# Performance work log

Hardware: AMD Instinct MI355X
Metric: run time of the kernel (lower is better)

Reference implementation:

```python
import jax, jax.numpy as jnp
import numpy as np

B, N, D = 2, 128, 512  # batch, tokens, embed_dim (= in_features = out_features)
LAYERS = 3


def setup_inputs() -> dict:
    key = jax.random.key(0)
    ks = jax.random.split(key, 9)
    s = lambda fan_in: 1.0 / np.sqrt(fan_in)
    return {
        "text_embedding": jax.random.normal(ks[0], (B, N, D), dtype=jnp.float32),
        # weights stored as [in, out] so y = x @ W + b (matches torch Linear math)
        "W_rel": jax.random.uniform(ks[1], (2 * D, D), jnp.float32, -s(2 * D), s(2 * D)),
        "b_rel": jax.random.uniform(ks[2], (D,), jnp.float32, -s(2 * D), s(2 * D)),
        "W_go": jax.random.uniform(ks[3], (D, D), jnp.float32, -s(D), s(D)),
        "b_go": jax.random.uniform(ks[4], (D,), jnp.float32, -s(D), s(D)),
        "W_gr": jax.random.uniform(ks[5], (3 * D, D), jnp.float32, -s(3 * D), s(3 * D)),
        "b_gr": jax.random.uniform(ks[6], (D,), jnp.float32, -s(3 * D), s(3 * D)),
        "W_esa": jax.random.uniform(ks[7], (D, D), jnp.float32, -s(D), s(D)),
        "b_esa": jax.random.uniform(ks[8], (D,), jnp.float32, -s(D), s(D)),
    }


def reference(text_embedding, W_rel, b_rel, W_go, b_go, W_gr, b_gr, W_esa, b_esa):
    x = text_embedding  # [B, N, D]
    n = x.shape[1]
    rel = None
    for i in range(LAYERS):
        new_x = jnp.tanh(x @ W_go + b_go)  # [B, N, D]
        # pairwise broadcast-concat: [B, N, N, 2D]
        a = jnp.broadcast_to(x[:, :, None, :], (x.shape[0], n, n, x.shape[-1]))
        b = jnp.broadcast_to(x[:, None, :, :], (x.shape[0], n, n, x.shape[-1]))
        rlf = jnp.concatenate([a, b], axis=3)
        if i == 0:
            rel = rlf @ W_rel + b_rel  # [B, N, N, D]
        rlf2 = jnp.concatenate([rlf, rel], axis=3)  # [B, N, N, 3D]
        rel = jnp.tanh(rlf2 @ W_gr + b_gr)  # [B, N, N, D]
        x = new_x
    rel = rel @ W_esa + b_esa  # [B, N, N, D]
    # original subtracts max over dim=1 then applies Softmax(dim=1); equivalent to stable softmax over axis 1
    attn = jax.nn.softmax(rel, axis=1)
    rel_out = jnp.sum(attn * rel, axis=-2)  # sum over second N axis -> [B, N, D]
    return (x, rel_out)
```

## Files before the change

kernel.cpp:

```cpp
#include <hip/hip_runtime.h>
#include <hip/hip_bf16.h>
#include <stdint.h>


#define DEV static __device__ __forceinline__

typedef float  f32x4   __attribute__((ext_vector_type(4)));
typedef float  f32x16  __attribute__((ext_vector_type(16)));
typedef __bf16 bf16x8  __attribute__((ext_vector_type(8)));
typedef __bf16 bf16x4  __attribute__((ext_vector_type(4)));

DEV float tanh_fast(float x) {
  float e = __expf(2.0f * x);
  return 1.0f - 2.0f * __frcp_rn(e + 1.0f);
}

DEV void gl_lds16(const void* g, void* l) {
  __builtin_amdgcn_global_load_lds(
      (const __attribute__((address_space(1))) unsigned int*)g,
      (__attribute__((address_space(3))) unsigned int*)l, 16, 0, 0);
}

struct WC { const float* W; __bf16* Wh; __bf16* Wl; };
struct Prep {
  WC w[7];
  const float* x0; __bf16* x0h; __bf16* x0l;
  const float* b_rel; const float* Wgrc; const float* b_gr; float* dvec;
};

__global__ __launch_bounds__(256) void prep_kernel(Prep pp) {
  const int y = blockIdx.y;
  if (y < 7) {
    const WC wc = pp.w[y];
    __shared__ float tile[32][33];
    int t = threadIdx.x;
    int tx = t & 31, ty = t >> 5;
    int bx = blockIdx.x & 15, by = blockIdx.x >> 4;
    int k0 = by * 32, n0 = bx * 32;
#pragma unroll
    for (int r = 0; r < 4; ++r) {
      int k = ty + r * 8;
      tile[k][tx] = wc.W[(size_t)(k0 + k) * 512 + n0 + tx];
    }
    __syncthreads();
#pragma unroll
    for (int r = 0; r < 4; ++r) {
      int n = ty + r * 8;
      float v = tile[tx][n];
      __bf16 h = (__bf16)v;
      wc.Wh[(size_t)(n0 + n) * 512 + k0 + tx] = h;
      wc.Wl[(size_t)(n0 + n) * 512 + k0 + tx] = (__bf16)(v - (float)h);
    }
  } else if (y == 7) {
    int i = blockIdx.x * 256 + threadIdx.x;
    if (i < 32768) {
      float4 v = ((const float4*)pp.x0)[i];
      float vv[4] = {v.x, v.y, v.z, v.w};
      bf16x4 h, l;
#pragma unroll
      for (int e = 0; e < 4; ++e) {
        __bf16 he = (__bf16)vv[e];
        h[e] = he;
        l[e] = (__bf16)(vv[e] - (float)he);
      }
      ((bf16x4*)pp.x0h)[i] = h;
      ((bf16x4*)pp.x0l)[i] = l;
    }
  } else {
    if (blockIdx.x < 2) {
      int n = blockIdx.x * 256 + threadIdx.x;
      float acc = pp.b_gr[n];
#pragma unroll 8
      for (int k = 0; k < 512; ++k) acc += pp.b_rel[k] * pp.Wgrc[(size_t)k * 512 + n];
      pp.dvec[n] = acc;
    }
  }
}

struct MOp {
  const __bf16* Xh; const __bf16* Xl;
  const __bf16* Wh; const __bf16* Wl;
  const float* bias;
  const float* add;
  float* outf;
  __bf16* outh; __bf16* outl;
  int act;
};
struct MBatch { MOp op[5]; };

__global__ __launch_bounds__(256, 2) void mfma_small_kernel(MBatch batch) {
  const MOp o = batch.op[blockIdx.y];
  const int m0 = ((int)blockIdx.x >> 3) * 64;
  const int n0 = ((int)blockIdx.x & 7) * 64;
  __shared__ __bf16 Ah[64 * 64], Al[64 * 64], Bh[64 * 64], Bl[64 * 64];
  const int t = threadIdx.x, lane = t & 63, wave = t >> 6;
  const int waveM = wave >> 1, waveN = wave & 1;
  const bool comp = (o.Xl != nullptr);

  f32x4 vzero = {0.f, 0.f, 0.f, 0.f};
  f32x4 acc[2][2];
#pragma unroll
  for (int a = 0; a < 2; ++a)
#pragma unroll
    for (int c = 0; c < 2; ++c) acc[a][c] = vzero;

  const int lr = lane >> 3, lc = (lane & 7) * 8;

  for (int k0 = 0; k0 < 512; k0 += 64) {
    __syncthreads();
#pragma unroll
    for (int r = 0; r < 2; ++r) {
      const int rb = r * 32 + wave * 8;
      gl_lds16(o.Xh + (size_t)(m0 + rb + lr) * 512 + k0 + lc, &Ah[rb * 64]);
      gl_lds16(o.Wh + (size_t)(n0 + rb + lr) * 512 + k0 + lc, &Bh[rb * 64]);
      if (comp) {
        gl_lds16(o.Xl + (size_t)(m0 + rb + lr) * 512 + k0 + lc, &Al[rb * 64]);
        gl_lds16(o.Wl + (size_t)(n0 + rb + lr) * 512 + k0 + lc, &Bl[rb * 64]);
      }
    }
    __syncthreads();
#pragma unroll
    for (int kk = 0; kk < 2; ++kk) {
      const int koff = kk * 32 + (lane >> 4) * 8;
      const int ml = lane & 15;
      bf16x8 ah[2], bh[2], al[2], bl[2];
#pragma unroll
      for (int tm = 0; tm < 2; ++tm)
        ah[tm] = *(const bf16x8*)&Ah[(waveM * 32 + tm * 16 + ml) * 64 + koff];
#pragma unroll
      for (int tn = 0; tn < 2; ++tn)
        bh[tn] = *(const bf16x8*)&Bh[(waveN * 32 + tn * 16 + ml) * 64 + koff];
      if (comp) {
#pragma unroll
        for (int tm = 0; tm < 2; ++tm)
          al[tm] = *(const bf16x8*)&Al[(waveM * 32 + tm * 16 + ml) * 64 + koff];
#pragma unroll
        for (int tn = 0; tn < 2; ++tn)
          bl[tn] = *(const bf16x8*)&Bl[(waveN * 32 + tn * 16 + ml) * 64 + koff];
      }
#pragma unroll
      for (int tm = 0; tm < 2; ++tm)
#pragma unroll
        for (int tn = 0; tn < 2; ++tn) {
          acc[tm][tn] = __builtin_amdgcn_mfma_f32_16x16x32_bf16(ah[tm], bh[tn], acc[tm][tn], 0, 0, 0);
          if (comp) {
            acc[tm][tn] = __builtin_amdgcn_mfma_f32_16x16x32_bf16(ah[tm], bl[tn], acc[tm][tn], 0, 0, 0);
            acc[tm][tn] = __builtin_amdgcn_mfma_f32_16x16x32_bf16(al[tm], bh[tn], acc[tm][tn], 0, 0, 0);
          }
        }
    }
  }

  const int quad = lane >> 4, cl = lane & 15;
#pragma unroll
  for (int tm = 0; tm < 2; ++tm) {
#pragma unroll
    for (int r = 0; r < 4; ++r) {
      const int row = m0 + waveM * 32 + tm * 16 + quad * 4 + r;
#pragma unroll
      for (int tn = 0; tn < 2; ++tn) {
        const int col = n0 + waveN * 32 + tn * 16 + cl;
        float v = acc[tm][tn][r];
        if (o.bias) v += o.bias[col];
        if (o.add) v += o.add[(size_t)row * 512 + col];
        if (o.act) v = tanh_fast(v);
        if (o.outf) o.outf[(size_t)row * 512 + col] = v;
        if (o.outh) {
          __bf16 h = (__bf16)v;
          o.outh[(size_t)row * 512 + col] = h;
          o.outl[(size_t)row * 512 + col] = (__bf16)(v - (float)h);
        }
      }
    }
  }
}

__global__ __launch_bounds__(256) void rel1_kernel(
    const float* __restrict__ A, const float* __restrict__ C,
    __bf16* __restrict__ R1) {
  size_t e = ((size_t)blockIdx.x * 256 + threadIdx.x) * 8;
  int d = (int)(e & 511);
  int j = (int)((e >> 9) & 127);
  int bi = (int)(e >> 16);
  int b = bi >> 7;
  const float* ap = &A[(size_t)bi * 512 + d];
  const float* cp = &C[((size_t)(b * 128 + j)) * 512 + d];
  float av[8], cv[8];
  *(float4*)&av[0] = *(const float4*)ap;
  *(float4*)&av[4] = *(const float4*)(ap + 4);
  *(float4*)&cv[0] = *(const float4*)cp;
  *(float4*)&cv[4] = *(const float4*)(cp + 4);
  bf16x8 o;
#pragma unroll
  for (int k = 0; k < 8; ++k) o[k] = (__bf16)tanh_fast(av[k] + cv[k]);
  *(bf16x8*)&R1[e] = o;
}

constexpr int BM = 128, BN = 128, BK = 64;
DEV int lds_off(int row) { return row * 64 + (row >> 3) * 8; }

template <int MODE>
__global__ __launch_bounds__(256, 2) void big_gemm_kernel(
    const __bf16* __restrict__ Ab, const __bf16* __restrict__ Wt,
    const float* __restrict__ P, const float* __restrict__ Q,
    const float* __restrict__ bias, __bf16* __restrict__ outb,
    float* __restrict__ outf) {
  __shared__ __bf16 As[BM * BK + 16 * 8];
  __shared__ __bf16 Bs[BN * BK + 16 * 8];
  const int t = threadIdx.x;
  const int lane = t & 63;
  const int wave = t >> 6;
  const int bm = (int)blockIdx.x >> 2;
  const int n0 = ((int)blockIdx.x & 3) * BN;
  const size_t r0 = (size_t)bm * BM;
  const int b = bm >> 7;
  const int i = bm & 127;
  const int waveM = wave >> 1, waveN = wave & 1;

  f32x16 acc[2][2];
#pragma unroll
  for (int a = 0; a < 2; ++a)
#pragma unroll
    for (int c = 0; c < 2; ++c) acc[a][c] = (f32x16)0.f;

  for (int k0 = 0; k0 < 512; k0 += BK) {
    __syncthreads();
#pragma unroll
    for (int p2 = 0; p2 < 4; ++p2) {
      int rowg = wave * 32 + p2 * 8;
      const __bf16* ga = Ab + (r0 + rowg + (lane >> 3)) * 512 + k0 + (lane & 7) * 8;
      gl_lds16(ga, &As[lds_off(rowg)]);
      const __bf16* gb = Wt + (size_t)(n0 + rowg + (lane >> 3)) * 512 + k0 + (lane & 7) * 8;
      gl_lds16(gb, &Bs[lds_off(rowg)]);
    }
    __syncthreads();
    const int ml = lane & 31;
    const int kl = (lane >> 5) * 8;
#pragma unroll
    for (int ks = 0; ks < 4; ++ks) {
      const int koff = ks * 16 + kl;
      bf16x8 af[2], bfr[2];
#pragma unroll
      for (int tm = 0; tm < 2; ++tm)
        af[tm] = *(const bf16x8*)&As[lds_off(waveM * 64 + tm * 32 + ml) + koff];
#pragma unroll
      for (int tn = 0; tn < 2; ++tn)
        bfr[tn] = *(const bf16x8*)&Bs[lds_off(waveN * 64 + tn * 32 + ml) + koff];
#pragma unroll
      for (int tm = 0; tm < 2; ++tm)
#pragma unroll
        for (int tn = 0; tn < 2; ++tn)
          acc[tm][tn] = __builtin_amdgcn_mfma_f32_32x32x16_bf16(af[tm], bfr[tn], acc[tm][tn], 0, 0, 0);
    }
  }

  const int cl = lane & 31, lg = lane >> 5;
#pragma unroll
  for (int tm = 0; tm < 2; ++tm) {
#pragma unroll
    for (int tn = 0; tn < 2; ++tn) {
      const int col = n0 + waveN * 64 + tn * 32 + cl;
      float pv;
      if (MODE == 2) pv = bias[col];
      else pv = P[((size_t)(b * 128 + i)) * 512 + col];
#pragma unroll
      for (int reg = 0; reg < 16; ++reg) {
        const int row = waveM * 64 + tm * 32 + (reg & 3) + 8 * (reg >> 2) + 4 * lg;
        float v = acc[tm][tn][reg] + pv;
        if (MODE == 2) {
          outf[(r0 + row) * 512 + col] = v;
        } else {
          v += Q[((size_t)(b * 128 + row)) * 512 + col];
          outb[(r0 + row) * 512 + col] = (__bf16)tanh_fast(v);
        }
      }
    }
  }
}

__global__ __launch_bounds__(256) void softmax_l_kernel(
    const float* __restrict__ S, float* __restrict__ Lb) {
  int idx = blockIdx.x * 256 + threadIdx.x;
  int d = idx & 511;
  int j = (idx >> 9) & 127;
  int b = idx >> 16;
  const float* p = S + ((size_t)b * 16384 + j) * 512 + d;
  float l = 0.f;
#pragma unroll 8
  for (int ii = 0; ii < 128; ++ii) l += __expf(p[(size_t)ii * 65536]);
  Lb[idx] = __frcp_rn(l);
}

__global__ __launch_bounds__(256) void softmax_out_kernel(
    const float* __restrict__ S, const float* __restrict__ Lb,
    float* __restrict__ outp) {
  int idx = blockIdx.x * 256 + threadIdx.x;
  int d = idx & 511;
  int i = (idx >> 9) & 127;
  int b = idx >> 16;
  const float* sp = S + ((size_t)(b * 128 + i)) * 65536 + d;
  const float* lp = Lb + (size_t)b * 65536 + d;
  float acc = 0.f;
#pragma unroll 8
  for (int jj = 0; jj < 128; ++jj) {
    float s = sp[(size_t)jj * 512];
    acc += __expf(s) * lp[(size_t)jj * 512] * s;
  }
  outp[idx] = acc;
}

extern "C" void kernel_launch(void* const* d_in, const int* in_sizes, int n_in,
                              void* d_out, int out_size, void* d_ws, size_t ws_size,
                              hipStream_t stream) {
  const float* x0    = (const float*)d_in[0];
  const float* W_rel = (const float*)d_in[1];
  const float* b_rel = (const float*)d_in[2];
  const float* W_go  = (const float*)d_in[3];
  const float* b_go  = (const float*)d_in[4];
  const float* W_gr  = (const float*)d_in[5];
  const float* b_gr  = (const float*)d_in[6];
  const float* W_esa = (const float*)d_in[7];
  const float* b_esa = (const float*)d_in[8];

  const float* Wrel_top = W_rel;
  const float* Wrel_bot = W_rel + 512 * 512;
  const float* Wgr_a = W_gr;
  const float* Wgr_b = W_gr + 512 * 512;
  const float* Wgr_c = W_gr + 2 * 512 * 512;

  char* ws = (char*)d_ws;
  size_t off = 0;
  auto alloc = [&](size_t bytes) -> void* {
    void* p = ws + off;
    off += (bytes + 255) & ~(size_t)255;
    return p;
  };
  const size_t NREL = 16777216ull;
  float*  S  = (float*)alloc(NREL * 4);
  __bf16* R1 = (__bf16*)alloc(NREL * 2);
  __bf16* R2 = (__bf16*)alloc(NREL * 2);
  float* p0t  = (float*)alloc(131072 * 4);
  float* q0t  = (float*)alloc(131072 * 4);
  float* Abuf = (float*)alloc(131072 * 4);
  float* Cbuf = (float*)alloc(131072 * 4);
  float* p1   = (float*)alloc(131072 * 4);
  float* q1   = (float*)alloc(131072 * 4);
  float* p2   = (float*)alloc(131072 * 4);
  float* q2   = (float*)alloc(131072 * 4);
  float* dvec = (float*)alloc(512 * 4);
  float* Lb   = (float*)alloc(131072 * 4);
  __bf16* x0h = (__bf16*)alloc(131072 * 2);
  __bf16* x0l = (__bf16*)alloc(131072 * 2);
  __bf16* x1h = (__bf16*)alloc(131072 * 2);
  __bf16* x1l = (__bf16*)alloc(131072 * 2);
  __bf16* x2h = (__bf16*)alloc(131072 * 2);
  __bf16* x2l = (__bf16*)alloc(131072 * 2);
  __bf16* u0h = (__bf16*)alloc(131072 * 2);
  __bf16* u0l = (__bf16*)alloc(131072 * 2);
  __bf16* v0h = (__bf16*)alloc(131072 * 2);
  __bf16* v0l = (__bf16*)alloc(131072 * 2);
  __bf16* Wgo_h = (__bf16*)alloc(262144 * 2);
  __bf16* Wgo_l = (__bf16*)alloc(262144 * 2);
  __bf16* Wrt_h = (__bf16*)alloc(262144 * 2);
  __bf16* Wrt_l = (__bf16*)alloc(262144 * 2);
  __bf16* Wrb_h = (__bf16*)alloc(262144 * 2);
  __bf16* Wrb_l = (__bf16*)alloc(262144 * 2);
  __bf16* Wga_h = (__bf16*)alloc(262144 * 2);
  __bf16* Wga_l = (__bf16*)alloc(262144 * 2);
  __bf16* Wgb_h = (__bf16*)alloc(262144 * 2);
  __bf16* Wgb_l = (__bf16*)alloc(262144 * 2);
  __bf16* Wgc_h = (__bf16*)alloc(262144 * 2);
  __bf16* Wgc_l = (__bf16*)alloc(262144 * 2);
  __bf16* Wes_h = (__bf16*)alloc(262144 * 2);
  __bf16* Wes_l = (__bf16*)alloc(262144 * 2);

  float* x3out  = (float*)d_out;
  float* relout = (float*)d_out + 131072;

  Prep pp;
  pp.w[0] = {W_go, Wgo_h, Wgo_l};
  pp.w[1] = {Wrel_top, Wrt_h, Wrt_l};
  pp.w[2] = {Wrel_bot, Wrb_h, Wrb_l};
  pp.w[3] = {Wgr_a, Wga_h, Wga_l};
  pp.w[4] = {Wgr_b, Wgb_h, Wgb_l};
  pp.w[5] = {Wgr_c, Wgc_h, Wgc_l};
  pp.w[6] = {W_esa, Wes_h, Wes_l};
  pp.x0 = x0; pp.x0h = x0h; pp.x0l = x0l;
  pp.b_rel = b_rel; pp.Wgrc = Wgr_c; pp.b_gr = b_gr; pp.dvec = dvec;
  prep_kernel<<<dim3(256, 9), 256, 0, stream>>>(pp);

  MBatch m1 = {};
  m1.op[0] = {x0h, x0l, Wgo_h, Wgo_l, b_go, nullptr, nullptr, x1h, x1l, 1};
  m1.op[1] = {x0h, x0l, Wrt_h, Wrt_l, nullptr, nullptr, nullptr, u0h, u0l, 0};
  m1.op[2] = {x0h, x0l, Wrb_h, Wrb_l, nullptr, nullptr, nullptr, v0h, v0l, 0};
  m1.op[3] = {x0h, x0l, Wga_h, Wga_l, nullptr, nullptr, p0t, nullptr, nullptr, 0};
  m1.op[4] = {x0h, x0l, Wgb_h, Wgb_l, nullptr, nullptr, q0t, nullptr, nullptr, 0};
  mfma_small_kernel<<<dim3(32, 5), 256, 0, stream>>>(m1);

  MBatch m2 = {};
  m2.op[0] = {x1h, x1l, Wgo_h, Wgo_l, b_go, nullptr, nullptr, x2h, x2l, 1};
  m2.op[1] = {u0h, u0l, Wgc_h, Wgc_l, dvec, p0t, Abuf, nullptr, nullptr, 0};
  m2.op[2] = {v0h, v0l, Wgc_h, Wgc_l, nullptr, q0t, Cbuf, nullptr, nullptr, 0};
  m2.op[3] = {x1h, x1l, Wga_h, Wga_l, b_gr, nullptr, p1, nullptr, nullptr, 0};
  m2.op[4] = {x1h, x1l, Wgb_h, Wgb_l, nullptr, nullptr, q1, nullptr, nullptr, 0};
  mfma_small_kernel<<<dim3(32, 5), 256, 0, stream>>>(m2);

  MBatch m3 = {};
  m3.op[0] = {x2h, x2l, Wgo_h, Wgo_l, b_go, nullptr, x3out, nullptr, nullptr, 1};
  m3.op[1] = {x2h, x2l, Wga_h, Wga_l, b_gr, nullptr, p2, nullptr, nullptr, 0};
  m3.op[2] = {x2h, x2l, Wgb_h, Wgb_l, nullptr, nullptr, q2, nullptr, nullptr, 0};
  mfma_small_kernel<<<dim3(32, 3), 256, 0, stream>>>(m3);

  rel1_kernel<<<8192, 256, 0, stream>>>(Abuf, Cbuf, R1);

  big_gemm_kernel<1><<<1024, 256, 0, stream>>>(R1, Wgc_h, p1, q1, nullptr, R2, nullptr);
  big_gemm_kernel<1><<<1024, 256, 0, stream>>>(R2, Wgc_h, p2, q2, nullptr, R1, nullptr);
  big_gemm_kernel<2><<<1024, 256, 0, stream>>>(R1, Wes_h, nullptr, nullptr, b_esa, nullptr, S);

  softmax_l_kernel<<<512, 256, 0, stream>>>(S, Lb);
  softmax_out_kernel<<<512, 256, 0, stream>>>(S, Lb, relout);
}
```

Baseline: 272.1 us.

## Fuse rel init and three pairwise GEMM layers into one LDS-resident chain kernel

Replaces the rel1 elementwise kernel and three separate big GEMM launches with one chain_kernel. Each block keeps a 128x512 bf16 rel tile in LDS across all three layers and writes only the final fp32 S to global memory. Weights are prearranged in the prep kernel into MFMA fragment order so they can be streamed straight from global/L2 into registers. This removes the round trips of the bf16 R1/R2 intermediates through HBM and two launches. In exchange, the grid drops to 256 blocks of 512 threads at one block per CU with large LDS use, so occupancy and latency hiding are lower.

```diff
diff --git a/kernel.cpp b/kernel.cpp
--- a/kernel.cpp
+++ b/kernel.cpp
@@ -23,17 +23,18 @@
 
 struct WC { const float* W; __bf16* Wh; __bf16* Wl; };
 struct Prep {
-  WC w[7];
+  WC w[6];
   const float* x0; __bf16* x0h; __bf16* x0l;
   const float* b_rel; const float* Wgrc; const float* b_gr; float* dvec;
+  const float* Wesa; __bf16* Wgcf; __bf16* Wesf;
 };
 
 __global__ __launch_bounds__(256) void prep_kernel(Prep pp) {
   const int y = blockIdx.y;
-  if (y < 7) {
+  const int t = threadIdx.x;
+  if (y < 6) {
     const WC wc = pp.w[y];
     __shared__ float tile[32][33];
-    int t = threadIdx.x;
     int tx = t & 31, ty = t >> 5;
     int bx = blockIdx.x & 15, by = blockIdx.x >> 4;
     int k0 = by * 32, n0 = bx * 32;
@@ -51,8 +52,8 @@
       wc.Wh[(size_t)(n0 + n) * 512 + k0 + tx] = h;
       wc.Wl[(size_t)(n0 + n) * 512 + k0 + tx] = (__bf16)(v - (float)h);
     }
-  } else if (y == 7) {
-    int i = blockIdx.x * 256 + threadIdx.x;
+  } else if (y == 6) {
+    int i = blockIdx.x * 256 + t;
     if (i < 32768) {
       float4 v = ((const float4*)pp.x0)[i];
       float vv[4] = {v.x, v.y, v.z, v.w};
@@ -66,13 +67,28 @@
       ((bf16x4*)pp.x0h)[i] = h;
       ((bf16x4*)pp.x0l)[i] = l;
     }
-  } else {
+  } else if (y == 7) {
     if (blockIdx.x < 2) {
-      int n = blockIdx.x * 256 + threadIdx.x;
+      int n = blockIdx.x * 256 + t;
       float acc = pp.b_gr[n];
 #pragma unroll 8
       for (int k = 0; k < 512; ++k) acc += pp.b_rel[k] * pp.Wgrc[(size_t)k * 512 + n];
       pp.dvec[n] = acc;
+    }
+  } else {
+    if (blockIdx.x < 128) {
+      const float* W = (y == 8) ? pp.Wgrc : pp.Wesa;
+      __bf16* Wf = (y == 8) ? pp.Wgcf : pp.Wesf;
+      int gid = blockIdx.x * 256 + t;
+      int lane = gid & 63;
+      int frag = gid >> 6;
+      int kt = frag & 31, nt = frag >> 5;
+      int n = nt * 32 + (lane & 31);
+      int k0 = kt * 16 + (lane >> 5) * 8;
+      bf16x8 o;
+#pragma unroll
+      for (int e = 0; e < 8; ++e) o[e] = (__bf16)W[(size_t)(k0 + e) * 512 + n];
+      *(bf16x8*)&Wf[(size_t)gid * 8] = o;
     }
   }
 }
@@ -175,103 +191,103 @@
   }
 }
 
-__global__ __launch_bounds__(256) void rel1_kernel(
-    const float* __restrict__ A, const float* __restrict__ C,
-    __bf16* __restrict__ R1) {
-  size_t e = ((size_t)blockIdx.x * 256 + threadIdx.x) * 8;
-  int d = (int)(e & 511);
-  int j = (int)((e >> 9) & 127);
-  int bi = (int)(e >> 16);
-  int b = bi >> 7;
-  const float* ap = &A[(size_t)bi * 512 + d];
-  const float* cp = &C[((size_t)(b * 128 + j)) * 512 + d];
-  float av[8], cv[8];
-  *(float4*)&av[0] = *(const float4*)ap;
-  *(float4*)&av[4] = *(const float4*)(ap + 4);
-  *(float4*)&cv[0] = *(const float4*)cp;
-  *(float4*)&cv[4] = *(const float4*)(cp + 4);
-  bf16x8 o;
-#pragma unroll
-  for (int k = 0; k < 8; ++k) o[k] = (__bf16)tanh_fast(av[k] + cv[k]);
-  *(bf16x8*)&R1[e] = o;
-}
-
-constexpr int BM = 128, BN = 128, BK = 64;
-DEV int lds_off(int row) { return row * 64 + (row >> 3) * 8; }
-
-template <int MODE>
-__global__ __launch_bounds__(256, 2) void big_gemm_kernel(
-    const __bf16* __restrict__ Ab, const __bf16* __restrict__ Wt,
-    const float* __restrict__ P, const float* __restrict__ Q,
-    const float* __restrict__ bias, __bf16* __restrict__ outb,
-    float* __restrict__ outf) {
-  __shared__ __bf16 As[BM * BK + 16 * 8];
-  __shared__ __bf16 Bs[BN * BK + 16 * 8];
+constexpr int RS = 520;
+
+__global__ __launch_bounds__(512, 1) void chain_kernel(
+    const float* __restrict__ Abuf, const float* __restrict__ Cbuf,
+    const __bf16* __restrict__ Wgcf, const __bf16* __restrict__ Wesf,
+    const float* __restrict__ p1, const float* __restrict__ q1,
+    const float* __restrict__ p2, const float* __restrict__ q2,
+    const float* __restrict__ b_esa, float* __restrict__ S) {
+  __shared__ __bf16 rel[128 * RS];
   const int t = threadIdx.x;
-  const int lane = t & 63;
-  const int wave = t >> 6;
-  const int bm = (int)blockIdx.x >> 2;
-  const int n0 = ((int)blockIdx.x & 3) * BN;
-  const size_t r0 = (size_t)bm * BM;
+  const int lane = t & 63, wave = t >> 6;
+  const int bm = blockIdx.x;
   const int b = bm >> 7;
-  const int i = bm & 127;
-  const int waveM = wave >> 1, waveN = wave & 1;
-
-  f32x16 acc[2][2];
-#pragma unroll
-  for (int a = 0; a < 2; ++a)
-#pragma unroll
-    for (int c = 0; c < 2; ++c) acc[a][c] = (f32x16)0.f;
-
-  for (int k0 = 0; k0 < 512; k0 += BK) {
-    __syncthreads();
-#pragma unroll
-    for (int p2 = 0; p2 < 4; ++p2) {
-      int rowg = wave * 32 + p2 * 8;
-      const __bf16* ga = Ab + (r0 + rowg + (lane >> 3)) * 512 + k0 + (lane & 7) * 8;
-      gl_lds16(ga, &As[lds_off(rowg)]);
-      const __bf16* gb = Wt + (size_t)(n0 + rowg + (lane >> 3)) * 512 + k0 + (lane & 7) * 8;
-      gl_lds16(gb, &Bs[lds_off(rowg)]);
-    }
-    __syncthreads();
-    const int ml = lane & 31;
-    const int kl = (lane >> 5) * 8;
-#pragma unroll
-    for (int ks = 0; ks < 4; ++ks) {
-      const int koff = ks * 16 + kl;
-      bf16x8 af[2], bfr[2];
-#pragma unroll
-      for (int tm = 0; tm < 2; ++tm)
-        af[tm] = *(const bf16x8*)&As[lds_off(waveM * 64 + tm * 32 + ml) + koff];
-#pragma unroll
-      for (int tn = 0; tn < 2; ++tn)
-        bfr[tn] = *(const bf16x8*)&Bs[lds_off(waveN * 64 + tn * 32 + ml) + koff];
-#pragma unroll
-      for (int tm = 0; tm < 2; ++tm)
-#pragma unroll
-        for (int tn = 0; tn < 2; ++tn)
-          acc[tm][tn] = __builtin_amdgcn_mfma_f32_32x32x16_bf16(af[tm], bfr[tn], acc[tm][tn], 0, 0, 0);
-    }
-  }
-
-  const int cl = lane & 31, lg = lane >> 5;
-#pragma unroll
-  for (int tm = 0; tm < 2; ++tm) {
-#pragma unroll
-    for (int tn = 0; tn < 2; ++tn) {
-      const int col = n0 + waveN * 64 + tn * 32 + cl;
-      float pv;
-      if (MODE == 2) pv = bias[col];
-      else pv = P[((size_t)(b * 128 + i)) * 512 + col];
-#pragma unroll
-      for (int reg = 0; reg < 16; ++reg) {
-        const int row = waveM * 64 + tm * 32 + (reg & 3) + 8 * (reg >> 2) + 4 * lg;
-        float v = acc[tm][tn][reg] + pv;
-        if (MODE == 2) {
-          outf[(r0 + row) * 512 + col] = v;
-        } else {
-          v += Q[((size_t)(b * 128 + row)) * 512 + col];
-          outb[(r0 + row) * 512 + col] = (__bf16)tanh_fast(v);
+
+  {
+    const int j = t >> 2, qt = (t & 3) * 128;
+    const float* ap = &Abuf[(size_t)bm * 512 + qt];
+    const float* cp = &Cbuf[((size_t)(b * 128 + j)) * 512 + qt];
+#pragma unroll
+    for (int c = 0; c < 128; c += 8) {
+      float4 a0 = *(const float4*)(ap + c), a1 = *(const float4*)(ap + c + 4);
+      float4 c0 = *(const float4*)(cp + c), c1 = *(const float4*)(cp + c + 4);
+      float av[8] = {a0.x + c0.x, a0.y + c0.y, a0.z + c0.z, a0.w + c0.w,
+                     a1.x + c1.x, a1.y + c1.y, a1.z + c1.z, a1.w + c1.w};
+      bf16x8 o;
+#pragma unroll
+      for (int e = 0; e < 8; ++e) o[e] = (__bf16)tanh_fast(av[e]);
+      *(bf16x8*)&rel[j * RS + qt + c] = o;
+    }
+  }
+  __syncthreads();
+
+  const int ml = lane & 31;
+  const int kg = (lane >> 5) * 8;
+  const int lg = lane >> 5;
+
+  for (int l = 0; l < 3; ++l) {
+    const __bf16* Wf = (l == 2) ? Wesf : Wgcf;
+    f32x16 acc[4][2];
+#pragma unroll
+    for (int a = 0; a < 4; ++a)
+#pragma unroll
+      for (int c = 0; c < 2; ++c) acc[a][c] = (f32x16)0.f;
+
+    const size_t fb0 = ((size_t)((wave * 2 + 0) * 32) * 64 + lane) * 8;
+    const size_t fb1 = ((size_t)((wave * 2 + 1) * 32) * 64 + lane) * 8;
+    bf16x8 b0 = *(const bf16x8*)&Wf[fb0];
+    bf16x8 b1 = *(const bf16x8*)&Wf[fb1];
+#pragma unroll 4
+    for (int kt = 0; kt < 32; ++kt) {
+      const int ktn = (kt + 1) & 31;
+      bf16x8 n0 = *(const bf16x8*)&Wf[fb0 + (size_t)ktn * 512];
+      bf16x8 n1 = *(const bf16x8*)&Wf[fb1 + (size_t)ktn * 512];
+      bf16x8 af[4];
+#pragma unroll
+      for (int tm = 0; tm < 4; ++tm)
+        af[tm] = *(const bf16x8*)&rel[(tm * 32 + ml) * RS + kt * 16 + kg];
+#pragma unroll
+      for (int tm = 0; tm < 4; ++tm) {
+        acc[tm][0] = __builtin_amdgcn_mfma_f32_32x32x16_bf16(af[tm], b0, acc[tm][0], 0, 0, 0);
+        acc[tm][1] = __builtin_amdgcn_mfma_f32_32x32x16_bf16(af[tm], b1, acc[tm][1], 0, 0, 0);
+      }
+      b0 = n0; b1 = n1;
+    }
+
+    if (l < 2) {
+      const float* P = l ? p2 : p1;
+      const float* Q = l ? q2 : q1;
+      __syncthreads();
+#pragma unroll
+      for (int tn = 0; tn < 2; ++tn) {
+        const int col = wave * 64 + tn * 32 + ml;
+        const float pv = P[(size_t)bm * 512 + col];
+#pragma unroll
+        for (int tm = 0; tm < 4; ++tm) {
+#pragma unroll
+          for (int reg = 0; reg < 16; ++reg) {
+            const int row = tm * 32 + (reg & 3) + 8 * (reg >> 2) + 4 * lg;
+            float v = acc[tm][tn][reg] + pv +
+                      Q[((size_t)(b * 128 + row)) * 512 + col];
+            rel[row * RS + col] = (__bf16)tanh_fast(v);
+          }
+        }
+      }
+      __syncthreads();
+    } else {
+#pragma unroll
+      for (int tn = 0; tn < 2; ++tn) {
+        const int col = wave * 64 + tn * 32 + ml;
+        const float bv = b_esa[col];
+#pragma unroll
+        for (int tm = 0; tm < 4; ++tm) {
+#pragma unroll
+          for (int reg = 0; reg < 16; ++reg) {
+            const int row = tm * 32 + (reg & 3) + 8 * (reg >> 2) + 4 * lg;
+            S[((size_t)bm * 128 + row) * 512 + col] = acc[tm][tn][reg] + bv;
+          }
         }
       }
     }
@@ -337,8 +353,6 @@
   };
   const size_t NREL = 16777216ull;
   float*  S  = (float*)alloc(NREL * 4);
-  __bf16* R1 = (__bf16*)alloc(NREL * 2);
-  __bf16* R2 = (__bf16*)alloc(NREL * 2);
   float* p0t  = (float*)alloc(131072 * 4);
   float* q0t  = (float*)alloc(131072 * 4);
   float* Abuf = (float*)alloc(131072 * 4);
@@ -371,8 +385,8 @@
   __bf16* Wgb_l = (__bf16*)alloc(262144 * 2);
   __bf16* Wgc_h = (__bf16*)alloc(262144 * 2);
   __bf16* Wgc_l = (__bf16*)alloc(262144 * 2);
-  __bf16* Wes_h = (__bf16*)alloc(262144 * 2);
-  __bf16* Wes_l = (__bf16*)alloc(262144 * 2);
+  __bf16* Wgcf  = (__bf16*)alloc(262144 * 2);
+  __bf16* Wesf  = (__bf16*)alloc(262144 * 2);
 
   float* x3out  = (float*)d_out;
   float* relout = (float*)d_out + 131072;
@@ -384,10 +398,10 @@
   pp.w[3] = {Wgr_a, Wga_h, Wga_l};
   pp.w[4] = {Wgr_b, Wgb_h, Wgb_l};
   pp.w[5] = {Wgr_c, Wgc_h, Wgc_l};
-  pp.w[6] = {W_esa, Wes_h, Wes_l};
   pp.x0 = x0; pp.x0h = x0h; pp.x0l = x0l;
   pp.b_rel = b_rel; pp.Wgrc = Wgr_c; pp.b_gr = b_gr; pp.dvec = dvec;
-  prep_kernel<<<dim3(256, 9), 256, 0, stream>>>(pp);
+  pp.Wesa = W_esa; pp.Wgcf = Wgcf; pp.Wesf = Wesf;
+  prep_kernel<<<dim3(256, 10), 256, 0, stream>>>(pp);
 
   MBatch m1 = {};
   m1.op[0] = {x0h, x0l, Wgo_h, Wgo_l, b_go, nullptr, nullptr, x1h, x1l, 1};
@@ -411,11 +425,8 @@
   m3.op[2] = {x2h, x2l, Wgb_h, Wgb_l, nullptr, nullptr, q2, nullptr, nullptr, 0};
   mfma_small_kernel<<<dim3(32, 3), 256, 0, stream>>>(m3);
 
-  rel1_kernel<<<8192, 256, 0, stream>>>(Abuf, Cbuf, R1);
-
-  big_gemm_kernel<1><<<1024, 256, 0, stream>>>(R1, Wgc_h, p1, q1, nullptr, R2, nullptr);
-  big_gemm_kernel<1><<<1024, 256, 0, stream>>>(R2, Wgc_h, p2, q2, nullptr, R1, nullptr);
-  big_gemm_kernel<2><<<1024, 256, 0, stream>>>(R1, Wes_h, nullptr, nullptr, b_esa, nullptr, S);
+  chain_kernel<<<256, 512, 0, stream>>>(Abuf, Cbuf, Wgcf, Wesf,
+                                        p1, q1, p2, q2, b_esa, S);
 
   softmax_l_kernel<<<512, 256, 0, stream>>>(S, Lb);
   softmax_out_kernel<<<512, 256, 0, stream>>>(S, Lb, relout);
```

Result: slower. 431.2 us (+58.5%).
